# Kernel optimization log

Measured on AMD Instinct MI355X. Metric: run time of the kernel, lower is better.

## Reference

```python
import jax, jax.numpy as jnp
import numpy as np

O, NI, F, D, NN, M = 2048, 16, 4, 128, 8, 8  # outfits, item slots, factors, dim, neighbors, valid slots
D2 = D // 2

def lrelu(x):
    return jax.nn.leaky_relu(x, 0.01)

def mlp2(x, W1, b1, W2, b2):
    # Linear -> LeakyReLU -> Linear -> LeakyReLU (Dropout is identity at inference)
    return lrelu(lrelu(x @ W1 + b1) @ W2 + b2)

def setup_inputs():
    ks = jax.random.split(jax.random.key(0), 16)
    s = 0.05
    pos = jnp.arange(NI)[None, :]
    outfit_items = jnp.where(pos < M, jax.random.randint(ks[0], (O, NI), 0, NI), -1)
    items_neighbor = jax.random.randint(ks[1], (O, NI, NN), -1, NI)
    items_feature = jax.random.normal(ks[2], (O, NI, D), dtype=jnp.float32)
    items_factors = jnp.zeros((O, NI, F, D), dtype=jnp.float32)
    p = {
        'cf_W1': jax.random.normal(ks[3], (F, D, D2)) * s,
        'cf_b1': jnp.zeros((F, D2)),
        'cf_W2': jax.random.normal(ks[4], (F, D2, D)) * s,
        'cf_b2': jnp.zeros((F, D)),
        'f2f_W1': jax.random.normal(ks[5], (D, D)) * s, 'f2f_b1': jnp.zeros((D,)),
        'f2f_W2': jax.random.normal(ks[6], (D, D)) * s, 'f2f_b2': jnp.zeros((D,)),
        'f2i_W1': jax.random.normal(ks[7], (D, D)) * s, 'f2i_b1': jnp.zeros((D,)),
        'f2i_W2': jax.random.normal(ks[8], (D, D)) * s, 'f2i_b2': jnp.zeros((D,)),
        'i2i_W1': jax.random.normal(ks[9], (D, D)) * s, 'i2i_b1': jnp.zeros((D,)),
        'i2i_W2': jax.random.normal(ks[10], (D, D)) * s, 'i2i_b2': jnp.zeros((D,)),
        'o2s_W': jax.random.normal(ks[11], (D, 1)) * s, 'o2s_b': jnp.zeros((1,)),
    }
    return dict(outfit_items=outfit_items, items_feature=items_feature,
                items_neighbor=items_neighbor, items_factors=items_factors, **p)

def _forward(outfit_items, items_feature, items_neighbor, items_factors,
             cf_W1, cf_b1, cf_W2, cf_b2, f2f_W1, f2f_b1, f2f_W2, f2f_b2,
             f2i_W1, f2i_b1, f2i_W2, f2i_b2, i2i_W1, i2i_b1, i2i_W2, i2i_b2,
             o2s_W, o2s_b):
    del items_factors  # creat_factors overwrites every entry in the original
    # --- creat_factors: per-factor 2-layer MLP on every item feature -> [O,NI,F,D]
    h = lrelu(jnp.einsum('oid,fde->oife', items_feature, cf_W1) + cf_b1)
    fac = lrelu(jnp.einsum('oife,fed->oifd', h, cf_W2) + cf_b2)

    # --- inter_factors: sequential over outfit slots; later slots read updated factors
    def outfit_fac(fac_o, oi_o, nbr_o):
        def step(f, i):
            valid = i != -1
            ic = jnp.maximum(i, 0)
            cand = jnp.concatenate([oi_o, nbr_o[ic]])                # [NI+NN]
            cm = (cand != -1) & (cand != i) & valid
            t = f[ic]                                                # [F,D] snapshot
            msg = mlp2(t[None] * f[jnp.maximum(cand, 0)],
                       f2f_W1, f2f_b1, f2f_W2, f2f_b2)               # [NI+NN,F,D]
            add = jnp.sum(jnp.where(cm[:, None, None], msg, 0.0), axis=0)
            return f.at[ic].add(jnp.where(valid, add, 0.0)), None
        f, _ = jax.lax.scan(step, fac_o, oi_o)
        return f
    fac = jax.vmap(outfit_fac)(fac, outfit_items, items_neighbor)

    # --- infer_items: feature[i] += sum_j f2i(fac[i,j]) for outfit members
    g = mlp2(fac, f2i_W1, f2i_b1, f2i_W2, f2i_b2).sum(axis=2)        # [O,NI,D]
    ic = jnp.maximum(outfit_items, 0)
    w = (outfit_items != -1).astype(g.dtype)                          # [O,NI]
    gsel = jnp.take_along_axis(g, ic[..., None], axis=1)
    scat = jax.vmap(lambda gs, idx, ww: jnp.zeros((NI, D), gs.dtype).at[idx].add(ww[:, None] * gs))
    feat = items_feature + scat(gsel, ic, w)

    # --- inter_items: sequential; current value detached (.data in original)
    def outfit_feat(fo_init, oi_o):
        jc = jnp.maximum(oi_o, 0)
        def step(fo, i):
            valid = i != -1
            ic_ = jnp.maximum(i, 0)
            t = jax.lax.stop_gradient(fo[ic_])
            msgs = mlp2(fo[jc], i2i_W1, i2i_b1, i2i_W2, i2i_b2)      # [NI,D]
            m = ((oi_o != -1) & (oi_o != i)).astype(fo.dtype)
            new = t + jnp.sum(m[:, None] * msgs, axis=0)
            return jnp.where(valid, fo.at[ic_].set(new), fo), None
        fo, _ = jax.lax.scan(step, fo_init, oi_o)
        return fo
    feat = jax.vmap(outfit_feat)(feat, outfit_items)

    # --- infer_outfit + score
    fsel = jnp.take_along_axis(feat, ic[..., None], axis=1)
    outfits = jnp.sum(w[..., None] * fsel, axis=1)                    # [O,D]
    scores = jax.nn.sigmoid(outfits @ o2s_W + o2s_b)[:, 0]            # [O]

    # --- com_loss: ||F F^T - I||_F^2 over valid slots (positional mask), / n_outfits
    G = jnp.einsum('oifd,oigd->oifg', fac, fac) - jnp.eye(F, dtype=fac.dtype)
    com = jnp.sum(w * jnp.sum(G * G, axis=(-1, -2))) / O
    return scores, jnp.reshape(com, (1,))

def reference(outfit_items, items_feature, items_neighbor, items_factors,
              cf_W1, cf_b1, cf_W2, cf_b2, f2f_W1, f2f_b1, f2f_W2, f2f_b2,
              f2i_W1, f2i_b1, f2i_W2, f2i_b2, i2i_W1, i2i_b1, i2i_W2, i2i_b2,
              o2s_W, o2s_b):
    return _forward(outfit_items, items_feature, items_neighbor, items_factors,
                    cf_W1, cf_b1, cf_W2, cf_b2, f2f_W1, f2f_b1, f2f_W2, f2f_b2,
                    f2i_W1, f2i_b1, f2i_W2, f2i_b2, i2i_W1, i2i_b1, i2i_W2, i2i_b2,
                    o2s_W, o2s_b)
```

## Files before the change

kernel.cpp:

```cpp
#include <hip/hip_runtime.h>
#include <math.h>


typedef __attribute__((ext_vector_type(8))) short short8;
typedef __attribute__((ext_vector_type(4))) float f32x4;

#define MFMA16(a, b, c) __builtin_amdgcn_mfma_f32_16x16x32_bf16(a, b, c, 0, 0, 0)

__device__ __forceinline__ float lrelu(float x) { return x > 0.0f ? x : 0.01f * x; }

__device__ __forceinline__ ushort f2bf(float f) {
  unsigned u = __builtin_bit_cast(unsigned, f);
  u += 0x7fffu + ((u >> 16) & 1u);
  return (ushort)(u >> 16);
}

__device__ __forceinline__ short8 load_bfrag(const float* __restrict__ W, int ldn,
                                             int kbase, int col) {
  short8 r;
#pragma unroll
  for (int j = 0; j < 8; ++j) r[j] = (short)f2bf(W[(kbase + j) * ldn + col]);
  return r;
}

__global__ void zero_com(float* out) { if (threadIdx.x == 0) out[2048] = 0.0f; }

__global__ __launch_bounds__(256, 2) void mfgn_kernel(
    const int* __restrict__ outfit_items,
    const float* __restrict__ items_feature,
    const int* __restrict__ items_neighbor,
    const float* __restrict__ cfW1, const float* __restrict__ cfb1,
    const float* __restrict__ cfW2, const float* __restrict__ cfb2,
    const float* __restrict__ f2fW1, const float* __restrict__ f2fb1,
    const float* __restrict__ f2fW2, const float* __restrict__ f2fb2,
    const float* __restrict__ f2iW1, const float* __restrict__ f2ib1,
    const float* __restrict__ f2iW2, const float* __restrict__ f2ib2,
    const float* __restrict__ i2iW1, const float* __restrict__ i2ib1,
    const float* __restrict__ i2iW2, const float* __restrict__ i2ib2,
    const float* __restrict__ o2sW, const float* __restrict__ o2sb,
    float* __restrict__ out)
{
  __shared__ float facL[16 * 528];
  __shared__ float featL[16 * 132];
  __shared__ ushort AB[64 * 136] __attribute__((aligned(16)));
  __shared__ float msgs[8 * 132];
  __shared__ float redE[16];
  __shared__ int oiL[16];
  __shared__ int nbrL[128];
  __shared__ int clAll[16 * 16];
  __shared__ int ncAll[16];
  __shared__ int vslL[16];
  __shared__ int refcntL[16];
  __shared__ int nvsL;

  const int o = blockIdx.x;
  const int tid = (int)threadIdx.x;
  const int lane = tid & 63;
  const int wid = tid >> 6;
  const int n16 = lane & 15;
  const int q = lane >> 4;
  const int kb = q * 8;

  if (tid < 16) oiL[tid] = outfit_items[o * 16 + tid];
  if (tid < 128) nbrL[tid] = items_neighbor[o * 128 + tid];
  {
    const int n = tid >> 4, d0 = (tid & 15) * 8;
    float4 a = *(const float4*)(items_feature + o * 2048 + tid * 8);
    float4 b = *(const float4*)(items_feature + o * 2048 + tid * 8 + 4);
    *(float4*)(featL + n * 132 + d0) = a;
    *(float4*)(featL + n * 132 + d0 + 4) = b;
    short8 pk;
    pk[0] = (short)f2bf(a.x); pk[1] = (short)f2bf(a.y);
    pk[2] = (short)f2bf(a.z); pk[3] = (short)f2bf(a.w);
    pk[4] = (short)f2bf(b.x); pk[5] = (short)f2bf(b.y);
    pk[6] = (short)f2bf(b.z); pk[7] = (short)f2bf(b.w);
    *(short8*)(AB + n * 136 + d0) = pk;
  }
  __syncthreads();

  if (tid == 0) {
    int cnt = 0;
    for (int s = 0; s < 16; ++s) refcntL[s] = 0;
    for (int s = 0; s < 16; ++s) {
      int v = oiL[s];
      if (v != -1) { vslL[cnt++] = s; refcntL[v]++; }
    }
    nvsL = cnt;
  }
  for (int s = wid; s < 16; s += 4) {
    const int iv = oiL[s];
    if (iv == -1) { if (lane == 0) ncAll[s] = 0; continue; }
    int cand = -1;
    if (lane < 24) cand = (lane < 16) ? oiL[lane] : nbrL[iv * 8 + (lane - 16)];
    bool ok = (lane < 24) && (cand != -1) && (cand != iv);
    unsigned long long bm = __ballot(ok);
    if (ok) clAll[s * 16 + __popcll(bm & ((1ull << lane) - 1ull))] = cand;
    if (lane == 0) ncAll[s] = (int)__popcll(bm);
  }
  __syncthreads();
  const int nvs = nvsL;

  {
    const int f = wid;
    f32x4 acc1[4];
#pragma unroll
    for (int nt = 0; nt < 4; ++nt) acc1[nt] = (f32x4){0.f, 0.f, 0.f, 0.f};
    for (int kt = 0; kt < 4; ++kt) {
      short8 a = *(const short8*)(AB + n16 * 136 + kt * 32 + kb);
#pragma unroll
      for (int nt = 0; nt < 4; ++nt) {
        short8 b = load_bfrag(cfW1 + f * 8192, 64, kt * 32 + kb, nt * 16 + n16);
        acc1[nt] = MFMA16(a, b, acc1[nt]);
      }
    }
    ushort* hidA = AB + 2176 + f * 1152;
#pragma unroll
    for (int nt = 0; nt < 4; ++nt)
#pragma unroll
      for (int r = 0; r < 4; ++r) {
        int item = q * 4 + r, e = nt * 16 + n16;
        hidA[item * 72 + e] = f2bf(lrelu(acc1[nt][r] + cfb1[f * 64 + e]));
      }
    f32x4 acc2[8];
#pragma unroll
    for (int nt = 0; nt < 8; ++nt) acc2[nt] = (f32x4){0.f, 0.f, 0.f, 0.f};
    for (int kt = 0; kt < 2; ++kt) {
      short8 a = *(const short8*)(hidA + n16 * 72 + kt * 32 + kb);
#pragma unroll
      for (int nt = 0; nt < 8; ++nt) {
        short8 b = load_bfrag(cfW2 + f * 8192, 128, kt * 32 + kb, nt * 16 + n16);
        acc2[nt] = MFMA16(a, b, acc2[nt]);
      }
    }
#pragma unroll
    for (int nt = 0; nt < 8; ++nt)
#pragma unroll
      for (int r = 0; r < 4; ++r) {
        int item = q * 4 + r, d = nt * 16 + n16;
        facL[item * 528 + f * 132 + d] = lrelu(acc2[nt][r] + cfb2[f * 128 + d]);
      }
  }
  __syncthreads();

  {
    const int ntg0 = wid * 2;
    const int col0 = ntg0 * 16 + n16, col1 = col0 + 16;
    short8 w1f[2][4], w2f[2][4];
#pragma unroll
    for (int ntl = 0; ntl < 2; ++ntl)
#pragma unroll
      for (int kt = 0; kt < 4; ++kt) {
        w1f[ntl][kt] = load_bfrag(f2fW1, 128, kt * 32 + kb, (ntg0 + ntl) * 16 + n16);
        w2f[ntl][kt] = load_bfrag(f2fW2, 128, kt * 32 + kb, (ntg0 + ntl) * 16 + n16);
      }
    const float b1v0 = f2fb1[col0], b1v1 = f2fb1[col1];
    const float b2v0 = f2fb2[col0], b2v1 = f2fb2[col1];

    for (int s = 0; s < 16; ++s) {
      const int iv = oiL[s];
      if (iv == -1) continue;
      const int nc = ncAll[s];
      {
        const int r = tid >> 2, kc = tid & 3;
        const int f = r & 3, ci = r >> 2;
        ushort* dst = AB + r * 136 + kc * 32;
        if (ci < nc) {
          const int cit = clAll[s * 16 + ci];
          const float* tp = facL + iv * 528 + f * 132 + kc * 32;
          const float* cp = facL + cit * 528 + f * 132 + kc * 32;
#pragma unroll
          for (int i = 0; i < 8; ++i) {
            float4 tv = *(const float4*)(tp + i * 4);
            float4 cv = *(const float4*)(cp + i * 4);
            ushort4 pk;
            pk.x = f2bf(tv.x * cv.x); pk.y = f2bf(tv.y * cv.y);
            pk.z = f2bf(tv.z * cv.z); pk.w = f2bf(tv.w * cv.w);
            *(ushort4*)(dst + i * 4) = pk;
          }
        } else {
          ushort4 z; z.x = z.y = z.z = z.w = 0;
#pragma unroll
          for (int i = 0; i < 8; ++i) *(ushort4*)(dst + i * 4) = z;
        }
      }
      __syncthreads();
      f32x4 acc[4][2];
#pragma unroll
      for (int mt = 0; mt < 4; ++mt) { acc[mt][0] = (f32x4){0.f,0.f,0.f,0.f}; acc[mt][1] = (f32x4){0.f,0.f,0.f,0.f}; }
      for (int kt = 0; kt < 4; ++kt)
#pragma unroll
        for (int mt = 0; mt < 4; ++mt) {
          short8 a = *(const short8*)(AB + (mt * 16 + n16) * 136 + kt * 32 + kb);
          acc[mt][0] = MFMA16(a, w1f[0][kt], acc[mt][0]);
          acc[mt][1] = MFMA16(a, w1f[1][kt], acc[mt][1]);
        }
      __syncthreads();
#pragma unroll
      for (int mt = 0; mt < 4; ++mt)
#pragma unroll
        for (int r = 0; r < 4; ++r) {
          int row = mt * 16 + q * 4 + r;
          AB[row * 136 + col0] = f2bf(lrelu(acc[mt][0][r] + b1v0));
          AB[row * 136 + col1] = f2bf(lrelu(acc[mt][1][r] + b1v1));
        }
      __syncthreads();
#pragma unroll
      for (int mt = 0; mt < 4; ++mt) { acc[mt][0] = (f32x4){0.f,0.f,0.f,0.f}; acc[mt][1] = (f32x4){0.f,0.f,0.f,0.f}; }
      for (int kt = 0; kt < 4; ++kt)
#pragma unroll
        for (int mt = 0; mt < 4; ++mt) {
          short8 a = *(const short8*)(AB + (mt * 16 + n16) * 136 + kt * 32 + kb);
          acc[mt][0] = MFMA16(a, w2f[0][kt], acc[mt][0]);
          acc[mt][1] = MFMA16(a, w2f[1][kt], acc[mt][1]);
        }
      float part[2][4];
#pragma unroll
      for (int ntl = 0; ntl < 2; ++ntl)
#pragma unroll
        for (int r = 0; r < 4; ++r) part[ntl][r] = 0.0f;
#pragma unroll
      for (int mt = 0; mt < 4; ++mt) {
        bool act = (mt * 4 + q) < nc;
#pragma unroll
        for (int r = 0; r < 4; ++r) {
          float y0 = lrelu(acc[mt][0][r] + b2v0);
          float y1 = lrelu(acc[mt][1][r] + b2v1);
          if (act) { part[0][r] += y0; part[1][r] += y1; }
        }
      }
#pragma unroll
      for (int ntl = 0; ntl < 2; ++ntl)
#pragma unroll
        for (int r = 0; r < 4; ++r) {
          float v = part[ntl][r];
          v += __shfl_xor(v, 16);
          v += __shfl_xor(v, 32);
          part[ntl][r] = v;
        }
      if (q == 0) {
#pragma unroll
        for (int r = 0; r < 4; ++r) {
          facL[iv * 528 + r * 132 + col0] += part[0][r];
          facL[iv * 528 + r * 132 + col1] += part[1][r];
        }
      }
      __syncthreads();
    }
  }

  {
    const int ntg0 = wid * 2;
    const int col0 = ntg0 * 16 + n16, col1 = col0 + 16;
    short8 w1f[2][4], w2f[2][4];
#pragma unroll
    for (int ntl = 0; ntl < 2; ++ntl)
#pragma unroll
      for (int kt = 0; kt < 4; ++kt) {
        w1f[ntl][kt] = load_bfrag(f2iW1, 128, kt * 32 + kb, (ntg0 + ntl) * 16 + n16);
        w2f[ntl][kt] = load_bfrag(f2iW2, 128, kt * 32 + kb, (ntg0 + ntl) * 16 + n16);
      }
    const float b1v0 = f2ib1[col0], b1v1 = f2ib1[col1];
    const float b2v0 = f2ib2[col0], b2v1 = f2ib2[col1];
    {
      const int r = tid >> 2, kc = tid & 3;
      const int f = r & 3, n = r >> 2;
      const float* sp = facL + n * 528 + f * 132 + kc * 32;
      ushort* dst = AB + r * 136 + kc * 32;
#pragma unroll
      for (int i = 0; i < 8; ++i) {
        float4 v = *(const float4*)(sp + i * 4);
        ushort4 pk;
        pk.x = f2bf(v.x); pk.y = f2bf(v.y); pk.z = f2bf(v.z); pk.w = f2bf(v.w);
        *(ushort4*)(dst + i * 4) = pk;
      }
    }
    __syncthreads();
    f32x4 acc[4][2];
#pragma unroll
    for (int mt = 0; mt < 4; ++mt) { acc[mt][0] = (f32x4){0.f,0.f,0.f,0.f}; acc[mt][1] = (f32x4){0.f,0.f,0.f,0.f}; }
    for (int kt = 0; kt < 4; ++kt)
#pragma unroll
      for (int mt = 0; mt < 4; ++mt) {
        short8 a = *(const short8*)(AB + (mt * 16 + n16) * 136 + kt * 32 + kb);
        acc[mt][0] = MFMA16(a, w1f[0][kt], acc[mt][0]);
        acc[mt][1] = MFMA16(a, w1f[1][kt], acc[mt][1]);
      }
    __syncthreads();
#pragma unroll
    for (int mt = 0; mt < 4; ++mt)
#pragma unroll
      for (int r = 0; r < 4; ++r) {
        int row = mt * 16 + q * 4 + r;
        AB[row * 136 + col0] = f2bf(lrelu(acc[mt][0][r] + b1v0));
        AB[row * 136 + col1] = f2bf(lrelu(acc[mt][1][r] + b1v1));
      }
    __syncthreads();
#pragma unroll
    for (int mt = 0; mt < 4; ++mt) { acc[mt][0] = (f32x4){0.f,0.f,0.f,0.f}; acc[mt][1] = (f32x4){0.f,0.f,0.f,0.f}; }
    for (int kt = 0; kt < 4; ++kt)
#pragma unroll
      for (int mt = 0; mt < 4; ++mt) {
        short8 a = *(const short8*)(AB + (mt * 16 + n16) * 136 + kt * 32 + kb);
        acc[mt][0] = MFMA16(a, w2f[0][kt], acc[mt][0]);
        acc[mt][1] = MFMA16(a, w2f[1][kt], acc[mt][1]);
      }
#pragma unroll
    for (int mt = 0; mt < 4; ++mt) {
      int item = mt * 4 + q;
      float g0 = 0.f, g1 = 0.f;
#pragma unroll
      for (int r = 0; r < 4; ++r) {
        g0 += lrelu(acc[mt][0][r] + b2v0);
        g1 += lrelu(acc[mt][1][r] + b2v1);
      }
      float rc = (float)refcntL[item];
      featL[item * 132 + col0] += rc * g0;
      featL[item * 132 + col1] += rc * g1;
    }
    __syncthreads();
  }

  {
    const int ntg0 = wid * 2;
    const int col0 = ntg0 * 16 + n16, col1 = col0 + 16;
    short8 w1f[2][4], w2f[2][4];
#pragma unroll
    for (int ntl = 0; ntl < 2; ++ntl)
#pragma unroll
      for (int kt = 0; kt < 4; ++kt) {
        w1f[ntl][kt] = load_bfrag(i2iW1, 128, kt * 32 + kb, (ntg0 + ntl) * 16 + n16);
        w2f[ntl][kt] = load_bfrag(i2iW2, 128, kt * 32 + kb, (ntg0 + ntl) * 16 + n16);
      }
    const float b1v0 = i2ib1[col0], b1v1 = i2ib1[col1];
    const float b2v0 = i2ib2[col0], b2v1 = i2ib2[col1];

    for (int u = 0; u < nvs; ++u) {
      const int iv = oiL[vslL[u]];
      {
        const int j = tid >> 5, kq = (tid & 31) * 4;
        if (j < nvs) {
          const int it = oiL[vslL[j]];
          float4 v = *(const float4*)(featL + it * 132 + kq);
          ushort4 pk;
          pk.x = f2bf(v.x); pk.y = f2bf(v.y); pk.z = f2bf(v.z); pk.w = f2bf(v.w);
          *(ushort4*)(AB + j * 136 + kq) = pk;
        }
      }
      __syncthreads();
      f32x4 acc[2];
      acc[0] = (f32x4){0.f,0.f,0.f,0.f}; acc[1] = (f32x4){0.f,0.f,0.f,0.f};
      for (int kt = 0; kt < 4; ++kt) {
        short8 a = *(const short8*)(AB + n16 * 136 + kt * 32 + kb);
        acc[0] = MFMA16(a, w1f[0][kt], acc[0]);
        acc[1] = MFMA16(a, w1f[1][kt], acc[1]);
      }
      __syncthreads();
#pragma unroll
      for (int r = 0; r < 4; ++r) {
        int row = q * 4 + r;
        AB[row * 136 + col0] = f2bf(lrelu(acc[0][r] + b1v0));
        AB[row * 136 + col1] = f2bf(lrelu(acc[1][r] + b1v1));
      }
      __syncthreads();
      acc[0] = (f32x4){0.f,0.f,0.f,0.f}; acc[1] = (f32x4){0.f,0.f,0.f,0.f};
      for (int kt = 0; kt < 4; ++kt) {
        short8 a = *(const short8*)(AB + n16 * 136 + kt * 32 + kb);
        acc[0] = MFMA16(a, w2f[0][kt], acc[0]);
        acc[1] = MFMA16(a, w2f[1][kt], acc[1]);
      }
      if (q < 2) {
#pragma unroll
        for (int r = 0; r < 4; ++r) {
          int j = q * 4 + r;
          msgs[j * 132 + col0] = lrelu(acc[0][r] + b2v0);
          msgs[j * 132 + col1] = lrelu(acc[1][r] + b2v1);
        }
      }
      __syncthreads();
      if (tid < 128) {
        float v = featL[iv * 132 + tid];
        for (int j = 0; j < nvs; ++j) {
          int it = oiL[vslL[j]];
          if (it != iv) v += msgs[j * 132 + tid];
        }
        featL[iv * 132 + tid] = v;
      }
      __syncthreads();
    }
  }

  if (tid < 128) {
    float sum = 0.0f;
    for (int u = 0; u < nvs; ++u) sum += featL[oiL[vslL[u]] * 132 + tid];
    float v = sum * o2sW[tid];
#pragma unroll
    for (int off = 1; off < 64; off <<= 1) v += __shfl_xor(v, off);
    if (lane == 0) redE[wid] = v;
  }
  __syncthreads();
  if (tid == 0) {
    float t = redE[0] + redE[1] + o2sb[0];
    out[o] = 1.0f / (1.0f + expf(-t));
  }
  __syncthreads();

  {
    const int n = tid >> 4, f = (tid >> 2) & 3, g = tid & 3;
    const float* pa = facL + n * 528 + f * 132;
    const float* pb = facL + n * 528 + g * 132;
    float dot = 0.0f;
    for (int i = 0; i < 32; ++i) {
      float4 a = *(const float4*)(pa + i * 4);
      float4 b = *(const float4*)(pb + i * 4);
      dot += a.x * b.x + a.y * b.y + a.z * b.z + a.w * b.w;
    }
    float v = dot - ((f == g) ? 1.0f : 0.0f);
    float sq = (oiL[n] != -1) ? v * v : 0.0f;
#pragma unroll
    for (int off = 1; off < 64; off <<= 1) sq += __shfl_xor(sq, off);
    if (lane == 0) redE[wid] = sq;
    __syncthreads();
    if (tid == 0) {
      float tot = redE[0] + redE[1] + redE[2] + redE[3];
      atomicAdd(out + 2048, tot * (1.0f / 2048.0f));
    }
  }
}

extern "C" void kernel_launch(void* const* d_in, const int* in_sizes, int n_in,
                              void* d_out, int out_size, void* d_ws, size_t ws_size,
                              hipStream_t stream) {
  float* out = (float*)d_out;
  hipLaunchKernelGGL(zero_com, dim3(1), dim3(64), 0, stream, out);
  hipLaunchKernelGGL(mfgn_kernel, dim3(2048), dim3(256), 0, stream,
                     (const int*)d_in[0],
                     (const float*)d_in[1],
                     (const int*)d_in[2],
                     (const float*)d_in[4], (const float*)d_in[5],
                     (const float*)d_in[6], (const float*)d_in[7],
                     (const float*)d_in[8], (const float*)d_in[9],
                     (const float*)d_in[10], (const float*)d_in[11],
                     (const float*)d_in[12], (const float*)d_in[13],
                     (const float*)d_in[14], (const float*)d_in[15],
                     (const float*)d_in[16], (const float*)d_in[17],
                     (const float*)d_in[18], (const float*)d_in[19],
                     (const float*)d_in[20], (const float*)d_in[21],
                     out);
}
```

Before: 393.7 us.

## Double block to 512 threads and split MFMA work across eight waves

Launches 512 threads per block instead of 256. All MLP stages are split across eight waves by M and N groups. Matmuls are transposed to use weights as the A operand, separate Xa/hidB buffers remove one barrier per stage, and conversions use packed bf16 intrinsics. Cross-wave factor updates now use shared atomicAdd. The aim is more parallelism inside each small per-outfit block, at the cost of higher register and LDS pressure and more idle waves in the i2i loop.

```diff
diff --git a/kernel.cpp b/kernel.cpp
--- a/kernel.cpp
+++ b/kernel.cpp
@@ -1,4 +1,5 @@
 #include <hip/hip_runtime.h>
+#include <hip/hip_bf16.h>
 #include <math.h>
 
 
@@ -15,6 +16,14 @@
   return (ushort)(u >> 16);
 }
 
+__device__ __forceinline__ unsigned pk2(float a, float b) {
+  float2 t; t.x = a; t.y = b;
+  __hip_bfloat162 h = __float22bfloat162_rn(t);
+  unsigned u;
+  __builtin_memcpy(&u, &h, 4);
+  return u;
+}
+
 __device__ __forceinline__ short8 load_bfrag(const float* __restrict__ W, int ldn,
                                              int kbase, int col) {
   short8 r;
@@ -25,7 +34,7 @@
 
 __global__ void zero_com(float* out) { if (threadIdx.x == 0) out[2048] = 0.0f; }
 
-__global__ __launch_bounds__(256, 2) void mfgn_kernel(
+__global__ __launch_bounds__(512, 4) void mfgn_kernel(
     const int* __restrict__ outfit_items,
     const float* __restrict__ items_feature,
     const int* __restrict__ items_neighbor,
@@ -42,9 +51,9 @@
 {
   __shared__ float facL[16 * 528];
   __shared__ float featL[16 * 132];
-  __shared__ ushort AB[64 * 136] __attribute__((aligned(16)));
-  __shared__ float msgs[8 * 132];
-  __shared__ float redE[16];
+  __shared__ ushort Xa[64 * 136] __attribute__((aligned(16)));
+  __shared__ ushort hidB[64 * 136] __attribute__((aligned(16)));
+  __shared__ float redE[8];
   __shared__ int oiL[16];
   __shared__ int nbrL[128];
   __shared__ int clAll[16 * 16];
@@ -57,6 +66,8 @@
   const int tid = (int)threadIdx.x;
   const int lane = tid & 63;
   const int wid = tid >> 6;
+  const int ng = wid & 3;
+  const int mg = wid >> 2;
   const int n16 = lane & 15;
   const int q = lane >> 4;
   const int kb = q * 8;
@@ -64,20 +75,12 @@
   if (tid < 16) oiL[tid] = outfit_items[o * 16 + tid];
   if (tid < 128) nbrL[tid] = items_neighbor[o * 128 + tid];
   {
-    const int n = tid >> 4, d0 = (tid & 15) * 8;
-    float4 a = *(const float4*)(items_feature + o * 2048 + tid * 8);
-    float4 b = *(const float4*)(items_feature + o * 2048 + tid * 8 + 4);
-    *(float4*)(featL + n * 132 + d0) = a;
-    *(float4*)(featL + n * 132 + d0 + 4) = b;
-    short8 pk;
-    pk[0] = (short)f2bf(a.x); pk[1] = (short)f2bf(a.y);
-    pk[2] = (short)f2bf(a.z); pk[3] = (short)f2bf(a.w);
-    pk[4] = (short)f2bf(b.x); pk[5] = (short)f2bf(b.y);
-    pk[6] = (short)f2bf(b.z); pk[7] = (short)f2bf(b.w);
-    *(short8*)(AB + n * 136 + d0) = pk;
-  }
-  __syncthreads();
-
+    const int n = tid >> 5, d0 = (tid & 31) * 4;
+    float4 v = *(const float4*)(items_feature + o * 2048 + tid * 4);
+    *(float4*)(featL + n * 132 + d0) = v;
+    uint2 pk; pk.x = pk2(v.x, v.y); pk.y = pk2(v.z, v.w);
+    *(uint2*)(Xa + n * 136 + d0) = pk;
+  }
   if (tid == 0) {
     int cnt = 0;
     for (int s = 0; s < 16; ++s) refcntL[s] = 0;
@@ -87,11 +90,12 @@
     }
     nvsL = cnt;
   }
-  for (int s = wid; s < 16; s += 4) {
-    const int iv = oiL[s];
+  for (int s = wid; s < 16; s += 8) {
+    const int iv = outfit_items[o * 16 + s];
     if (iv == -1) { if (lane == 0) ncAll[s] = 0; continue; }
     int cand = -1;
-    if (lane < 24) cand = (lane < 16) ? oiL[lane] : nbrL[iv * 8 + (lane - 16)];
+    if (lane < 24) cand = (lane < 16) ? outfit_items[o * 16 + lane]
+                                      : items_neighbor[o * 128 + iv * 8 + (lane - 16)];
     bool ok = (lane < 24) && (cand != -1) && (cand != iv);
     unsigned long long bm = __ballot(ok);
     if (ok) clAll[s * 16 + __popcll(bm & ((1ull << lane) - 1ull))] = cand;
@@ -101,117 +105,129 @@
   const int nvs = nvsL;
 
   {
-    const int f = wid;
-    f32x4 acc1[4];
-#pragma unroll
-    for (int nt = 0; nt < 4; ++nt) acc1[nt] = (f32x4){0.f, 0.f, 0.f, 0.f};
+    const int f = wid & 3, half = wid >> 2;
+    short8 wA[2][4];
+#pragma unroll
+    for (int etl = 0; etl < 2; ++etl)
+#pragma unroll
+      for (int kt = 0; kt < 4; ++kt)
+        wA[etl][kt] = load_bfrag(cfW1 + f * 8192, 64, kt * 32 + kb, (half * 2 + etl) * 16 + n16);
+    f32x4 acc[2];
+    acc[0] = (f32x4){0.f,0.f,0.f,0.f}; acc[1] = (f32x4){0.f,0.f,0.f,0.f};
     for (int kt = 0; kt < 4; ++kt) {
-      short8 a = *(const short8*)(AB + n16 * 136 + kt * 32 + kb);
-#pragma unroll
-      for (int nt = 0; nt < 4; ++nt) {
-        short8 b = load_bfrag(cfW1 + f * 8192, 64, kt * 32 + kb, nt * 16 + n16);
-        acc1[nt] = MFMA16(a, b, acc1[nt]);
-      }
-    }
-    ushort* hidA = AB + 2176 + f * 1152;
-#pragma unroll
-    for (int nt = 0; nt < 4; ++nt)
-#pragma unroll
-      for (int r = 0; r < 4; ++r) {
-        int item = q * 4 + r, e = nt * 16 + n16;
-        hidA[item * 72 + e] = f2bf(lrelu(acc1[nt][r] + cfb1[f * 64 + e]));
-      }
-    f32x4 acc2[8];
-#pragma unroll
-    for (int nt = 0; nt < 8; ++nt) acc2[nt] = (f32x4){0.f, 0.f, 0.f, 0.f};
+      short8 x = *(const short8*)(Xa + n16 * 136 + kt * 32 + kb);
+      acc[0] = MFMA16(wA[0][kt], x, acc[0]);
+      acc[1] = MFMA16(wA[1][kt], x, acc[1]);
+    }
+#pragma unroll
+    for (int etl = 0; etl < 2; ++etl) {
+      f32x4 b1q = *(const f32x4*)(cfb1 + f * 64 + (half * 2 + etl) * 16 + q * 4);
+      float h0 = lrelu(acc[etl][0] + b1q[0]), h1 = lrelu(acc[etl][1] + b1q[1]);
+      float h2 = lrelu(acc[etl][2] + b1q[2]), h3 = lrelu(acc[etl][3] + b1q[3]);
+      uint2 pk; pk.x = pk2(h0, h1); pk.y = pk2(h2, h3);
+      *(uint2*)(hidB + (f * 16 + n16) * 136 + (half * 2 + etl) * 16 + q * 4) = pk;
+    }
+    __syncthreads();
+    short8 wB[4][2];
+#pragma unroll
+    for (int ctl = 0; ctl < 4; ++ctl)
+#pragma unroll
+      for (int kt = 0; kt < 2; ++kt)
+        wB[ctl][kt] = load_bfrag(cfW2 + f * 8192, 128, kt * 32 + kb, half * 64 + ctl * 16 + n16);
+    f32x4 acc2[4];
+#pragma unroll
+    for (int ctl = 0; ctl < 4; ++ctl) acc2[ctl] = (f32x4){0.f,0.f,0.f,0.f};
     for (int kt = 0; kt < 2; ++kt) {
-      short8 a = *(const short8*)(hidA + n16 * 72 + kt * 32 + kb);
-#pragma unroll
-      for (int nt = 0; nt < 8; ++nt) {
-        short8 b = load_bfrag(cfW2 + f * 8192, 128, kt * 32 + kb, nt * 16 + n16);
-        acc2[nt] = MFMA16(a, b, acc2[nt]);
-      }
-    }
-#pragma unroll
-    for (int nt = 0; nt < 8; ++nt)
-#pragma unroll
-      for (int r = 0; r < 4; ++r) {
-        int item = q * 4 + r, d = nt * 16 + n16;
-        facL[item * 528 + f * 132 + d] = lrelu(acc2[nt][r] + cfb2[f * 128 + d]);
-      }
-  }
-  __syncthreads();
-
-  {
-    const int ntg0 = wid * 2;
-    const int col0 = ntg0 * 16 + n16, col1 = col0 + 16;
+      short8 h = *(const short8*)(hidB + (f * 16 + n16) * 136 + kt * 32 + kb);
+#pragma unroll
+      for (int ctl = 0; ctl < 4; ++ctl) acc2[ctl] = MFMA16(h, wB[ctl][kt], acc2[ctl]);
+    }
+#pragma unroll
+    for (int ctl = 0; ctl < 4; ++ctl) {
+      int c = half * 64 + ctl * 16 + n16;
+      float b2 = cfb2[f * 128 + c];
+#pragma unroll
+      for (int r = 0; r < 4; ++r)
+        facL[(q * 4 + r) * 528 + f * 132 + c] = lrelu(acc2[ctl][r] + b2);
+    }
+    __syncthreads();
+  }
+
+  {
     short8 w1f[2][4], w2f[2][4];
 #pragma unroll
     for (int ntl = 0; ntl < 2; ++ntl)
 #pragma unroll
       for (int kt = 0; kt < 4; ++kt) {
-        w1f[ntl][kt] = load_bfrag(f2fW1, 128, kt * 32 + kb, (ntg0 + ntl) * 16 + n16);
-        w2f[ntl][kt] = load_bfrag(f2fW2, 128, kt * 32 + kb, (ntg0 + ntl) * 16 + n16);
-      }
-    const float b1v0 = f2fb1[col0], b1v1 = f2fb1[col1];
-    const float b2v0 = f2fb2[col0], b2v1 = f2fb2[col1];
+        w1f[ntl][kt] = load_bfrag(f2fW1, 128, kt * 32 + kb, (ng * 2 + ntl) * 16 + n16);
+        w2f[ntl][kt] = load_bfrag(f2fW2, 128, kt * 32 + kb, (ng * 2 + ntl) * 16 + n16);
+      }
+    f32x4 b1q[2];
+    float b2v[2];
+#pragma unroll
+    for (int ntl = 0; ntl < 2; ++ntl) {
+      b1q[ntl] = *(const f32x4*)(f2fb1 + (ng * 2 + ntl) * 16 + q * 4);
+      b2v[ntl] = f2fb2[(ng * 2 + ntl) * 16 + n16];
+    }
+    const int rS = tid >> 3, kcS = tid & 7;
+    const int fS = rS & 3, ciS = rS >> 2;
+    const int k0 = kcS * 16;
 
     for (int s = 0; s < 16; ++s) {
       const int iv = oiL[s];
       if (iv == -1) continue;
       const int nc = ncAll[s];
-      {
-        const int r = tid >> 2, kc = tid & 3;
-        const int f = r & 3, ci = r >> 2;
-        ushort* dst = AB + r * 136 + kc * 32;
-        if (ci < nc) {
-          const int cit = clAll[s * 16 + ci];
-          const float* tp = facL + iv * 528 + f * 132 + kc * 32;
-          const float* cp = facL + cit * 528 + f * 132 + kc * 32;
-#pragma unroll
-          for (int i = 0; i < 8; ++i) {
-            float4 tv = *(const float4*)(tp + i * 4);
-            float4 cv = *(const float4*)(cp + i * 4);
-            ushort4 pk;
-            pk.x = f2bf(tv.x * cv.x); pk.y = f2bf(tv.y * cv.y);
-            pk.z = f2bf(tv.z * cv.z); pk.w = f2bf(tv.w * cv.w);
-            *(ushort4*)(dst + i * 4) = pk;
-          }
-        } else {
-          ushort4 z; z.x = z.y = z.z = z.w = 0;
-#pragma unroll
-          for (int i = 0; i < 8; ++i) *(ushort4*)(dst + i * 4) = z;
-        }
-      }
-      __syncthreads();
-      f32x4 acc[4][2];
-#pragma unroll
-      for (int mt = 0; mt < 4; ++mt) { acc[mt][0] = (f32x4){0.f,0.f,0.f,0.f}; acc[mt][1] = (f32x4){0.f,0.f,0.f,0.f}; }
+      if (ciS < nc) {
+        const int cit = clAll[s * 16 + ciS];
+        const float* tp = facL + iv * 528 + fS * 132;
+        const float* cp = facL + cit * 528 + fS * 132;
+#pragma unroll
+        for (int i2 = 0; i2 < 2; ++i2) {
+          const int k = k0 + i2 * 8;
+          float4 a0 = *(const float4*)(tp + k), a1 = *(const float4*)(tp + k + 4);
+          float4 c0 = *(const float4*)(cp + k), c1 = *(const float4*)(cp + k + 4);
+          uint4 u;
+          u.x = pk2(a0.x * c0.x, a0.y * c0.y); u.y = pk2(a0.z * c0.z, a0.w * c0.w);
+          u.z = pk2(a1.x * c1.x, a1.y * c1.y); u.w = pk2(a1.z * c1.z, a1.w * c1.w);
+          *(uint4*)(Xa + rS * 136 + k) = u;
+        }
+      } else {
+        uint4 z; z.x = z.y = z.z = z.w = 0;
+        *(uint4*)(Xa + rS * 136 + k0) = z;
+        *(uint4*)(Xa + rS * 136 + k0 + 8) = z;
+      }
+      __syncthreads();
+      f32x4 acc[2][2];
+#pragma unroll
+      for (int mt = 0; mt < 2; ++mt) { acc[mt][0] = (f32x4){0.f,0.f,0.f,0.f}; acc[mt][1] = (f32x4){0.f,0.f,0.f,0.f}; }
       for (int kt = 0; kt < 4; ++kt)
 #pragma unroll
-        for (int mt = 0; mt < 4; ++mt) {
-          short8 a = *(const short8*)(AB + (mt * 16 + n16) * 136 + kt * 32 + kb);
-          acc[mt][0] = MFMA16(a, w1f[0][kt], acc[mt][0]);
-          acc[mt][1] = MFMA16(a, w1f[1][kt], acc[mt][1]);
-        }
-      __syncthreads();
-#pragma unroll
-      for (int mt = 0; mt < 4; ++mt)
-#pragma unroll
-        for (int r = 0; r < 4; ++r) {
-          int row = mt * 16 + q * 4 + r;
-          AB[row * 136 + col0] = f2bf(lrelu(acc[mt][0][r] + b1v0));
-          AB[row * 136 + col1] = f2bf(lrelu(acc[mt][1][r] + b1v1));
-        }
-      __syncthreads();
-#pragma unroll
-      for (int mt = 0; mt < 4; ++mt) { acc[mt][0] = (f32x4){0.f,0.f,0.f,0.f}; acc[mt][1] = (f32x4){0.f,0.f,0.f,0.f}; }
+        for (int mt = 0; mt < 2; ++mt) {
+          short8 x = *(const short8*)(Xa + (mg * 32 + mt * 16 + n16) * 136 + kt * 32 + kb);
+          acc[mt][0] = MFMA16(w1f[0][kt], x, acc[mt][0]);
+          acc[mt][1] = MFMA16(w1f[1][kt], x, acc[mt][1]);
+        }
+#pragma unroll
+      for (int mt = 0; mt < 2; ++mt)
+#pragma unroll
+        for (int ntl = 0; ntl < 2; ++ntl) {
+          float h0 = lrelu(acc[mt][ntl][0] + b1q[ntl][0]);
+          float h1 = lrelu(acc[mt][ntl][1] + b1q[ntl][1]);
+          float h2 = lrelu(acc[mt][ntl][2] + b1q[ntl][2]);
+          float h3 = lrelu(acc[mt][ntl][3] + b1q[ntl][3]);
+          uint2 pk; pk.x = pk2(h0, h1); pk.y = pk2(h2, h3);
+          *(uint2*)(hidB + (mg * 32 + mt * 16 + n16) * 136 + (ng * 2 + ntl) * 16 + q * 4) = pk;
+        }
+      __syncthreads();
+      f32x4 acc2[2][2];
+#pragma unroll
+      for (int mt = 0; mt < 2; ++mt) { acc2[mt][0] = (f32x4){0.f,0.f,0.f,0.f}; acc2[mt][1] = (f32x4){0.f,0.f,0.f,0.f}; }
       for (int kt = 0; kt < 4; ++kt)
 #pragma unroll
-        for (int mt = 0; mt < 4; ++mt) {
-          short8 a = *(const short8*)(AB + (mt * 16 + n16) * 136 + kt * 32 + kb);
-          acc[mt][0] = MFMA16(a, w2f[0][kt], acc[mt][0]);
-          acc[mt][1] = MFMA16(a, w2f[1][kt], acc[mt][1]);
+        for (int mt = 0; mt < 2; ++mt) {
+          short8 h = *(const short8*)(hidB + (mg * 32 + mt * 16 + n16) * 136 + kt * 32 + kb);
+          acc2[mt][0] = MFMA16(h, w2f[0][kt], acc2[mt][0]);
+          acc2[mt][1] = MFMA16(h, w2f[1][kt], acc2[mt][1]);
         }
       float part[2][4];
 #pragma unroll
@@ -219,14 +235,14 @@
 #pragma unroll
         for (int r = 0; r < 4; ++r) part[ntl][r] = 0.0f;
 #pragma unroll
-      for (int mt = 0; mt < 4; ++mt) {
-        bool act = (mt * 4 + q) < nc;
-#pragma unroll
-        for (int r = 0; r < 4; ++r) {
-          float y0 = lrelu(acc[mt][0][r] + b2v0);
-          float y1 = lrelu(acc[mt][1][r] + b2v1);
-          if (act) { part[0][r] += y0; part[1][r] += y1; }
-        }
+      for (int mt = 0; mt < 2; ++mt) {
+        bool act = (mg * 8 + mt * 4 + q) < nc;
+        if (act)
+#pragma unroll
+          for (int ntl = 0; ntl < 2; ++ntl)
+#pragma unroll
+            for (int r = 0; r < 4; ++r)
+              part[ntl][r] += lrelu(acc2[mt][ntl][r] + b2v[ntl]);
       }
 #pragma unroll
       for (int ntl = 0; ntl < 2; ++ntl)
@@ -239,151 +255,172 @@
         }
       if (q == 0) {
 #pragma unroll
-        for (int r = 0; r < 4; ++r) {
-          facL[iv * 528 + r * 132 + col0] += part[0][r];
-          facL[iv * 528 + r * 132 + col1] += part[1][r];
-        }
-      }
-      __syncthreads();
-    }
-  }
-
-  {
-    const int ntg0 = wid * 2;
-    const int col0 = ntg0 * 16 + n16, col1 = col0 + 16;
+        for (int ntl = 0; ntl < 2; ++ntl)
+#pragma unroll
+          for (int r = 0; r < 4; ++r)
+            atomicAdd(&facL[iv * 528 + r * 132 + (ng * 2 + ntl) * 16 + n16], part[ntl][r]);
+      }
+      __syncthreads();
+    }
+  }
+
+  {
     short8 w1f[2][4], w2f[2][4];
 #pragma unroll
     for (int ntl = 0; ntl < 2; ++ntl)
 #pragma unroll
       for (int kt = 0; kt < 4; ++kt) {
-        w1f[ntl][kt] = load_bfrag(f2iW1, 128, kt * 32 + kb, (ntg0 + ntl) * 16 + n16);
-        w2f[ntl][kt] = load_bfrag(f2iW2, 128, kt * 32 + kb, (ntg0 + ntl) * 16 + n16);
-      }
-    const float b1v0 = f2ib1[col0], b1v1 = f2ib1[col1];
-    const float b2v0 = f2ib2[col0], b2v1 = f2ib2[col1];
+        w1f[ntl][kt] = load_bfrag(f2iW1, 128, kt * 32 + kb, (ng * 2 + ntl) * 16 + n16);
+        w2f[ntl][kt] = load_bfrag(f2iW2, 128, kt * 32 + kb, (ng * 2 + ntl) * 16 + n16);
+      }
+    f32x4 b1q[2];
+    float b2v[2];
+#pragma unroll
+    for (int ntl = 0; ntl < 2; ++ntl) {
+      b1q[ntl] = *(const f32x4*)(f2ib1 + (ng * 2 + ntl) * 16 + q * 4);
+      b2v[ntl] = f2ib2[(ng * 2 + ntl) * 16 + n16];
+    }
     {
-      const int r = tid >> 2, kc = tid & 3;
-      const int f = r & 3, n = r >> 2;
-      const float* sp = facL + n * 528 + f * 132 + kc * 32;
-      ushort* dst = AB + r * 136 + kc * 32;
-#pragma unroll
-      for (int i = 0; i < 8; ++i) {
-        float4 v = *(const float4*)(sp + i * 4);
-        ushort4 pk;
-        pk.x = f2bf(v.x); pk.y = f2bf(v.y); pk.z = f2bf(v.z); pk.w = f2bf(v.w);
-        *(ushort4*)(dst + i * 4) = pk;
-      }
-    }
-    __syncthreads();
-    f32x4 acc[4][2];
-#pragma unroll
-    for (int mt = 0; mt < 4; ++mt) { acc[mt][0] = (f32x4){0.f,0.f,0.f,0.f}; acc[mt][1] = (f32x4){0.f,0.f,0.f,0.f}; }
+      const int r = tid >> 3, kc = tid & 7, k0 = kc * 16;
+      const int f = r & 3, item = r >> 2;
+      const float* sp = facL + item * 528 + f * 132;
+#pragma unroll
+      for (int i2 = 0; i2 < 2; ++i2) {
+        const int k = k0 + i2 * 8;
+        float4 a0 = *(const float4*)(sp + k), a1 = *(const float4*)(sp + k + 4);
+        uint4 u;
+        u.x = pk2(a0.x, a0.y); u.y = pk2(a0.z, a0.w);
+        u.z = pk2(a1.x, a1.y); u.w = pk2(a1.z, a1.w);
+        *(uint4*)(Xa + r * 136 + k) = u;
+      }
+    }
+    __syncthreads();
+    f32x4 acc[2][2];
+#pragma unroll
+    for (int mt = 0; mt < 2; ++mt) { acc[mt][0] = (f32x4){0.f,0.f,0.f,0.f}; acc[mt][1] = (f32x4){0.f,0.f,0.f,0.f}; }
     for (int kt = 0; kt < 4; ++kt)
 #pragma unroll
-      for (int mt = 0; mt < 4; ++mt) {
-        short8 a = *(const short8*)(AB + (mt * 16 + n16) * 136 + kt * 32 + kb);
-        acc[mt][0] = MFMA16(a, w1f[0][kt], acc[mt][0]);
-        acc[mt][1] = MFMA16(a, w1f[1][kt], acc[mt][1]);
-      }
-    __syncthreads();
-#pragma unroll
-    for (int mt = 0; mt < 4; ++mt)
-#pragma unroll
-      for (int r = 0; r < 4; ++r) {
-        int row = mt * 16 + q * 4 + r;
-        AB[row * 136 + col0] = f2bf(lrelu(acc[mt][0][r] + b1v0));
-        AB[row * 136 + col1] = f2bf(lrelu(acc[mt][1][r] + b1v1));
-      }
-    __syncthreads();
-#pragma unroll
-    for (int mt = 0; mt < 4; ++mt) { acc[mt][0] = (f32x4){0.f,0.f,0.f,0.f}; acc[mt][1] = (f32x4){0.f,0.f,0.f,0.f}; }
+      for (int mt = 0; mt < 2; ++mt) {
+        short8 x = *(const short8*)(Xa + (mg * 32 + mt * 16 + n16) * 136 + kt * 32 + kb);
+        acc[mt][0] = MFMA16(w1f[0][kt], x, acc[mt][0]);
+        acc[mt][1] = MFMA16(w1f[1][kt], x, acc[mt][1]);
+      }
+#pragma unroll
+    for (int mt = 0; mt < 2; ++mt)
+#pragma unroll
+      for (int ntl = 0; ntl < 2; ++ntl) {
+        float h0 = lrelu(acc[mt][ntl][0] + b1q[ntl][0]);
+        float h1 = lrelu(acc[mt][ntl][1] + b1q[ntl][1]);
+        float h2 = lrelu(acc[mt][ntl][2] + b1q[ntl][2]);
+        float h3 = lrelu(acc[mt][ntl][3] + b1q[ntl][3]);
+        uint2 pk; pk.x = pk2(h0, h1); pk.y = pk2(h2, h3);
+        *(uint2*)(hidB + (mg * 32 + mt * 16 + n16) * 136 + (ng * 2 + ntl) * 16 + q * 4) = pk;
+      }
+    __syncthreads();
+    f32x4 acc2[2][2];
+#pragma unroll
+    for (int mt = 0; mt < 2; ++mt) { acc2[mt][0] = (f32x4){0.f,0.f,0.f,0.f}; acc2[mt][1] = (f32x4){0.f,0.f,0.f,0.f}; }
     for (int kt = 0; kt < 4; ++kt)
 #pragma unroll
-      for (int mt = 0; mt < 4; ++mt) {
-        short8 a = *(const short8*)(AB + (mt * 16 + n16) * 136 + kt * 32 + kb);
-        acc[mt][0] = MFMA16(a, w2f[0][kt], acc[mt][0]);
-        acc[mt][1] = MFMA16(a, w2f[1][kt], acc[mt][1]);
-      }
-#pragma unroll
-    for (int mt = 0; mt < 4; ++mt) {
-      int item = mt * 4 + q;
-      float g0 = 0.f, g1 = 0.f;
-#pragma unroll
-      for (int r = 0; r < 4; ++r) {
-        g0 += lrelu(acc[mt][0][r] + b2v0);
-        g1 += lrelu(acc[mt][1][r] + b2v1);
-      }
+      for (int mt = 0; mt < 2; ++mt) {
+        short8 h = *(const short8*)(hidB + (mg * 32 + mt * 16 + n16) * 136 + kt * 32 + kb);
+        acc2[mt][0] = MFMA16(h, w2f[0][kt], acc2[mt][0]);
+        acc2[mt][1] = MFMA16(h, w2f[1][kt], acc2[mt][1]);
+      }
+#pragma unroll
+    for (int mt = 0; mt < 2; ++mt) {
+      int item = mg * 8 + mt * 4 + q;
       float rc = (float)refcntL[item];
-      featL[item * 132 + col0] += rc * g0;
-      featL[item * 132 + col1] += rc * g1;
-    }
-    __syncthreads();
-  }
-
-  {
-    const int ntg0 = wid * 2;
-    const int col0 = ntg0 * 16 + n16, col1 = col0 + 16;
+#pragma unroll
+      for (int ntl = 0; ntl < 2; ++ntl) {
+        float g = 0.f;
+#pragma unroll
+        for (int r = 0; r < 4; ++r) g += lrelu(acc2[mt][ntl][r] + b2v[ntl]);
+        featL[item * 132 + (ng * 2 + ntl) * 16 + n16] += rc * g;
+      }
+    }
+    __syncthreads();
+  }
+
+  {
     short8 w1f[2][4], w2f[2][4];
 #pragma unroll
     for (int ntl = 0; ntl < 2; ++ntl)
 #pragma unroll
       for (int kt = 0; kt < 4; ++kt) {
-        w1f[ntl][kt] = load_bfrag(i2iW1, 128, kt * 32 + kb, (ntg0 + ntl) * 16 + n16);
-        w2f[ntl][kt] = load_bfrag(i2iW2, 128, kt * 32 + kb, (ntg0 + ntl) * 16 + n16);
-      }
-    const float b1v0 = i2ib1[col0], b1v1 = i2ib1[col1];
-    const float b2v0 = i2ib2[col0], b2v1 = i2ib2[col1];
+        w1f[ntl][kt] = load_bfrag(i2iW1, 128, kt * 32 + kb, (ng * 2 + ntl) * 16 + n16);
+        w2f[ntl][kt] = load_bfrag(i2iW2, 128, kt * 32 + kb, (ng * 2 + ntl) * 16 + n16);
+      }
+    f32x4 b1q[2];
+    float b2v[2];
+#pragma unroll
+    for (int ntl = 0; ntl < 2; ++ntl) {
+      b1q[ntl] = *(const f32x4*)(i2ib1 + (ng * 2 + ntl) * 16 + q * 4);
+      b2v[ntl] = i2ib2[(ng * 2 + ntl) * 16 + n16];
+    }
+    const int rS = tid >> 3, kcS = tid & 7, k0 = kcS * 16;
 
     for (int u = 0; u < nvs; ++u) {
       const int iv = oiL[vslL[u]];
-      {
-        const int j = tid >> 5, kq = (tid & 31) * 4;
-        if (j < nvs) {
-          const int it = oiL[vslL[j]];
-          float4 v = *(const float4*)(featL + it * 132 + kq);
-          ushort4 pk;
-          pk.x = f2bf(v.x); pk.y = f2bf(v.y); pk.z = f2bf(v.z); pk.w = f2bf(v.w);
-          *(ushort4*)(AB + j * 136 + kq) = pk;
-        }
-      }
-      __syncthreads();
-      f32x4 acc[2];
-      acc[0] = (f32x4){0.f,0.f,0.f,0.f}; acc[1] = (f32x4){0.f,0.f,0.f,0.f};
-      for (int kt = 0; kt < 4; ++kt) {
-        short8 a = *(const short8*)(AB + n16 * 136 + kt * 32 + kb);
-        acc[0] = MFMA16(a, w1f[0][kt], acc[0]);
-        acc[1] = MFMA16(a, w1f[1][kt], acc[1]);
-      }
-      __syncthreads();
-#pragma unroll
-      for (int r = 0; r < 4; ++r) {
-        int row = q * 4 + r;
-        AB[row * 136 + col0] = f2bf(lrelu(acc[0][r] + b1v0));
-        AB[row * 136 + col1] = f2bf(lrelu(acc[1][r] + b1v1));
-      }
-      __syncthreads();
-      acc[0] = (f32x4){0.f,0.f,0.f,0.f}; acc[1] = (f32x4){0.f,0.f,0.f,0.f};
-      for (int kt = 0; kt < 4; ++kt) {
-        short8 a = *(const short8*)(AB + n16 * 136 + kt * 32 + kb);
-        acc[0] = MFMA16(a, w2f[0][kt], acc[0]);
-        acc[1] = MFMA16(a, w2f[1][kt], acc[1]);
-      }
-      if (q < 2) {
-#pragma unroll
-        for (int r = 0; r < 4; ++r) {
-          int j = q * 4 + r;
-          msgs[j * 132 + col0] = lrelu(acc[0][r] + b2v0);
-          msgs[j * 132 + col1] = lrelu(acc[1][r] + b2v1);
-        }
-      }
-      __syncthreads();
-      if (tid < 128) {
-        float v = featL[iv * 132 + tid];
-        for (int j = 0; j < nvs; ++j) {
-          int it = oiL[vslL[j]];
-          if (it != iv) v += msgs[j * 132 + tid];
-        }
-        featL[iv * 132 + tid] = v;
+      if (rS < nvs) {
+        const int it = oiL[vslL[rS]];
+        const float* sp = featL + it * 132;
+#pragma unroll
+        for (int i2 = 0; i2 < 2; ++i2) {
+          const int k = k0 + i2 * 8;
+          float4 a0 = *(const float4*)(sp + k), a1 = *(const float4*)(sp + k + 4);
+          uint4 uu;
+          uu.x = pk2(a0.x, a0.y); uu.y = pk2(a0.z, a0.w);
+          uu.z = pk2(a1.x, a1.y); uu.w = pk2(a1.z, a1.w);
+          *(uint4*)(Xa + rS * 136 + k) = uu;
+        }
+      }
+      __syncthreads();
+      if (mg == 0) {
+        f32x4 acc[2];
+        acc[0] = (f32x4){0.f,0.f,0.f,0.f}; acc[1] = (f32x4){0.f,0.f,0.f,0.f};
+        for (int kt = 0; kt < 4; ++kt) {
+          short8 x = *(const short8*)(Xa + n16 * 136 + kt * 32 + kb);
+          acc[0] = MFMA16(w1f[0][kt], x, acc[0]);
+          acc[1] = MFMA16(w1f[1][kt], x, acc[1]);
+        }
+#pragma unroll
+        for (int ntl = 0; ntl < 2; ++ntl) {
+          float h0 = lrelu(acc[ntl][0] + b1q[ntl][0]);
+          float h1 = lrelu(acc[ntl][1] + b1q[ntl][1]);
+          float h2 = lrelu(acc[ntl][2] + b1q[ntl][2]);
+          float h3 = lrelu(acc[ntl][3] + b1q[ntl][3]);
+          uint2 pk; pk.x = pk2(h0, h1); pk.y = pk2(h2, h3);
+          *(uint2*)(hidB + n16 * 136 + (ng * 2 + ntl) * 16 + q * 4) = pk;
+        }
+      }
+      __syncthreads();
+      if (mg == 0) {
+        f32x4 acc2[2];
+        acc2[0] = (f32x4){0.f,0.f,0.f,0.f}; acc2[1] = (f32x4){0.f,0.f,0.f,0.f};
+        for (int kt = 0; kt < 4; ++kt) {
+          short8 h = *(const short8*)(hidB + n16 * 136 + kt * 32 + kb);
+          acc2[0] = MFMA16(h, w2f[0][kt], acc2[0]);
+          acc2[1] = MFMA16(h, w2f[1][kt], acc2[1]);
+        }
+        float part[2] = {0.f, 0.f};
+        if (q < 2) {
+#pragma unroll
+          for (int r = 0; r < 4; ++r) {
+            int j = q * 4 + r;
+            bool m = (j < nvs) && (oiL[vslL[j]] != iv);
+            if (m) {
+              part[0] += lrelu(acc2[0][r] + b2v[0]);
+              part[1] += lrelu(acc2[1][r] + b2v[1]);
+            }
+          }
+        }
+        part[0] += __shfl_xor(part[0], 16);
+        part[1] += __shfl_xor(part[1], 16);
+        if (q == 0) {
+          featL[iv * 132 + (ng * 2 + 0) * 16 + n16] += part[0];
+          featL[iv * 132 + (ng * 2 + 1) * 16 + n16] += part[1];
+        }
       }
       __syncthreads();
     }
@@ -402,26 +439,29 @@
     float t = redE[0] + redE[1] + o2sb[0];
     out[o] = 1.0f / (1.0f + expf(-t));
   }
-  __syncthreads();
-
-  {
-    const int n = tid >> 4, f = (tid >> 2) & 3, g = tid & 3;
-    const float* pa = facL + n * 528 + f * 132;
-    const float* pb = facL + n * 528 + g * 132;
+
+  {
+    const int n = tid >> 5, f = (tid >> 3) & 3, g = (tid >> 1) & 3, h = tid & 1;
+    const float* pa = facL + n * 528 + f * 132 + h * 64;
+    const float* pb = facL + n * 528 + g * 132 + h * 64;
     float dot = 0.0f;
-    for (int i = 0; i < 32; ++i) {
+    for (int i = 0; i < 16; ++i) {
       float4 a = *(const float4*)(pa + i * 4);
       float4 b = *(const float4*)(pb + i * 4);
       dot += a.x * b.x + a.y * b.y + a.z * b.z + a.w * b.w;
     }
+    dot += __shfl_xor(dot, 1);
     float v = dot - ((f == g) ? 1.0f : 0.0f);
-    float sq = (oiL[n] != -1) ? v * v : 0.0f;
+    float sq = (h == 0 && oiL[n] != -1) ? v * v : 0.0f;
 #pragma unroll
     for (int off = 1; off < 64; off <<= 1) sq += __shfl_xor(sq, off);
+    __syncthreads();
     if (lane == 0) redE[wid] = sq;
     __syncthreads();
     if (tid == 0) {
-      float tot = redE[0] + redE[1] + redE[2] + redE[3];
+      float tot = 0.f;
+#pragma unroll
+      for (int w = 0; w < 8; ++w) tot += redE[w];
       atomicAdd(out + 2048, tot * (1.0f / 2048.0f));
     }
   }
@@ -432,7 +472,7 @@
                               hipStream_t stream) {
   float* out = (float*)d_out;
   hipLaunchKernelGGL(zero_com, dim3(1), dim3(64), 0, stream, out);
-  hipLaunchKernelGGL(mfgn_kernel, dim3(2048), dim3(256), 0, stream,
+  hipLaunchKernelGGL(mfgn_kernel, dim3(2048), dim3(512), 0, stream,
                      (const int*)d_in[0],
                      (const float*)d_in[1],
                      (const int*)d_in[2],
```

Result: slower. 508.6 us (+29.2%).
